# Performance work log

Measured on AMD Instinct MI355X. Metric: run time of the kernel, lower is better.

## Reference

```python
import jax, jax.numpy as jnp
import numpy as np


def segment_softmax(logits, seg, num_seg):
    m = jax.ops.segment_max(logits, seg, num_segments=num_seg)
    z = jnp.exp(logits - m[seg])
    s = jax.ops.segment_sum(z, seg, num_segments=num_seg)
    return z / s[seg]


def hconv(x_lin, edge_node, edge_he, num_nodes, num_edges, bias, alpha=None):
    # PyG HypergraphConv (heads=1, concat=True): D^-1 H W_e B^-1 H^T X Theta
    ones = jnp.ones(edge_node.shape[0], x_lin.dtype)
    D = jax.ops.segment_sum(ones, edge_node, num_segments=num_nodes)
    Dinv = jnp.where(D > 0, 1.0 / D, 0.0)
    Bd = jax.ops.segment_sum(ones, edge_he, num_segments=num_edges)
    Binv = jnp.where(Bd > 0, 1.0 / Bd, 0.0)
    # node -> hyperedge
    msg = Binv[edge_he][:, None] * x_lin[edge_node]
    if alpha is not None:
        msg = alpha[:, None] * msg
    e = jax.ops.segment_sum(msg, edge_he, num_segments=num_edges)
    # hyperedge -> node
    msg2 = Dinv[edge_node][:, None] * e[edge_he]
    if alpha is not None:
        msg2 = alpha[:, None] * msg2
    out = jax.ops.segment_sum(msg2, edge_node, num_segments=num_nodes)
    return out + bias


def reference(c_it, medicine_it, c_embeddings, m_embeddings, W_conv, b_conv, W_gat, att, b_gat, he_attr):
    nd = c_embeddings.shape[0]  # all indicators are 1 -> nonzero indexing is identity
    nm = m_embeddings.shape[0]
    oc = W_conv.shape[0]

    # diagnosis hypergraph: single hyperedge containing all diseases
    dia_x = c_embeddings @ W_conv.T  # [nd, oc]
    dia_nf = hconv(dia_x, jnp.arange(nd), jnp.zeros(nd, jnp.int32), nd, 1, b_conv)

    # medicine hypergraph: single hyperedge containing all medicines
    med_x = m_embeddings @ W_conv.T  # [nm, oc]
    med_nf = hconv(med_x, jnp.arange(nm), jnp.zeros(nm, jnp.int32), nm, 1, b_conv)

    # dia-med hypergraph: nd hyperedges, hyperedge d = {disease d} U {all medicines}
    comb = jnp.concatenate([c_embeddings, m_embeddings], axis=0)  # [nd+nm, in]
    x_lin = comb @ W_gat.T                                        # [nd+nm, oc]
    he_lin = he_attr @ W_gat.T                                    # [nd, oc]
    med_nodes = jnp.arange(nd, nd + nm)
    edge_node = jnp.concatenate(
        [jnp.arange(nd)[:, None], jnp.broadcast_to(med_nodes[None, :], (nd, nm))], axis=1
    ).reshape(-1)                              # [nd*(nm+1)]
    edge_he = jnp.repeat(jnp.arange(nd), nm + 1)

    # attention (attention_mode='node'): alpha from source node + hyperedge attr, softmax per hyperedge
    a_node = x_lin @ att[:oc]   # [nd+nm]
    a_he = he_lin @ att[oc:]    # [nd]
    logits = jax.nn.leaky_relu(a_node[edge_node] + a_he[edge_he], 0.2)
    alpha = segment_softmax(logits, edge_he, nd)

    dm_nf = hconv(x_lin, edge_node, edge_he, nd + nm, nd, b_gat, alpha)  # [nd+nm, oc]

    disease_final = jnp.concatenate([dm_nf[:nd], dia_nf], axis=1)   # [nd, 2*oc]
    medicine_final = jnp.concatenate([dm_nf[nd:], med_nf], axis=1)  # [nm, 2*oc]
    return jnp.concatenate([disease_final, medicine_final], axis=0)  # [nd+nm, 2*oc]


def setup_inputs() -> dict:
    key = jax.random.key(0)
    ks = jax.random.split(key, 8)
    ND, NM, IN, OUT = 2048, 512, 256, 128
    s = 0.05
    return {
        "c_it": jnp.ones((ND,), jnp.int32),
        "medicine_it": jnp.ones((NM,), jnp.int32),
        "c_embeddings": jax.random.normal(ks[0], (ND, IN), jnp.float32),
        "m_embeddings": jax.random.normal(ks[1], (NM, IN), jnp.float32),
        "W_conv": jax.random.normal(ks[2], (OUT, IN), jnp.float32) * s,
        "b_conv": jax.random.normal(ks[3], (OUT,), jnp.float32) * s,
        "W_gat": jax.random.normal(ks[4], (OUT, IN), jnp.float32) * s,
        "att": jax.random.normal(ks[5], (2 * OUT,), jnp.float32) * s,
        "b_gat": jax.random.normal(ks[6], (OUT,), jnp.float32) * s,
        "he_attr": jax.random.normal(ks[7], (ND, IN), jnp.float32),
    }
```

## Files before the change

### kernel.cpp

```cpp
#include <hip/hip_runtime.h>

#define ND 2048
#define NM 512
#define DIN 256
#define OC 128
#define NTOT 2560
#define NE 513

#define WS_PARTC 0
#define WS_PARTM (WS_PARTC + 512*256)
#define WS_AHE   (WS_PARTM + 128*256)
#define WS_ANODE (WS_AHE + ND)
#define WS_XLIN  (WS_ANODE + NTOT)
#define WS_DIA   (WS_XLIN + NTOT*OC)
#define WS_MED   (WS_DIA + OC)
#define WS_PART2 (WS_MED + OC)

__device__ __forceinline__ float lrelu(float x) { return x > 0.f ? x : 0.2f * x; }

__global__ void __launch_bounds__(256) K1(
        const float* __restrict__ c_emb, const float* __restrict__ m_emb,
        const float* __restrict__ W_gat, const float* __restrict__ att,
        const float* __restrict__ he_attr, float* __restrict__ ws) {
    const int b = blockIdx.x, t = threadIdx.x;
    if (b < 640) {
        __shared__ float row[4][DIN];
        __shared__ float sA[4][OC];
        const int d0 = b * 4;
#pragma unroll
        for (int p = 0; p < 2; ++p) {
            const int idx = p * 256 + t;
            const int r = idx >> 7, c = idx & 127;
            const int d = d0 + r;
            const float* src = (d < ND) ? c_emb + (size_t)d * DIN
                                        : m_emb + (size_t)(d - ND) * DIN;
            const float2 u = ((const float2*)src)[c];
            row[r][2 * c]     = u.x;
            row[r][2 * c + 1] = u.y;
        }
        __syncthreads();
        {
            const float pc = row[0][t] + row[1][t] + row[2][t] + row[3][t];
            if (b < 512) ws[WS_PARTC + b * 256 + t] = pc;
            else         ws[WS_PARTM + (b - 512) * 256 + t] = pc;
        }
        const int o = t & (OC - 1), h = t >> 7;
        float a0 = 0.f, a1 = 0.f;
        const float4* wr = (const float4*)(W_gat + (size_t)o * DIN);
        const float* r0 = row[2 * h];
        const float* r1 = row[2 * h + 1];
#pragma unroll 8
        for (int v = 0; v < 64; ++v) {
            const float4 w = wr[v];
            const int ib = 4 * v;
            a0 = fmaf(r0[ib],     w.x, a0);
            a0 = fmaf(r0[ib + 1], w.y, a0);
            a0 = fmaf(r0[ib + 2], w.z, a0);
            a0 = fmaf(r0[ib + 3], w.w, a0);
            a1 = fmaf(r1[ib],     w.x, a1);
            a1 = fmaf(r1[ib + 1], w.y, a1);
            a1 = fmaf(r1[ib + 2], w.z, a1);
            a1 = fmaf(r1[ib + 3], w.w, a1);
        }
        ws[WS_XLIN + (size_t)(d0 + 2 * h) * OC + o]     = a0;
        ws[WS_XLIN + (size_t)(d0 + 2 * h + 1) * OC + o] = a1;
        const float at = att[o];
        sA[2 * h][o]     = a0 * at;
        sA[2 * h + 1][o] = a1 * at;
        __syncthreads();
#pragma unroll
        for (int st = 64; st >= 1; st >>= 1) {
            if (t < 4 * st) {
                const int r = t / st, i = t - r * st;
                sA[r][i] += sA[r][i + st];
            }
            __syncthreads();
        }
        if (t < 4) ws[WS_ANODE + d0 + t] = sA[t][0];
    } else {
        __shared__ float satt[OC];
        __shared__ float we[DIN];
        const int q = b - 640;
        if (t < OC) satt[t] = att[OC + t];
        __syncthreads();
        float acc = 0.f;
#pragma unroll 8
        for (int o = 0; o < OC; ++o)
            acc = fmaf(W_gat[(size_t)o * DIN + t], satt[o], acc);
        we[t] = acc;
        __syncthreads();
        const int r = t >> 5, l = t & 31;
        const int d = q * 8 + r;
        const float* he = he_attr + (size_t)d * DIN;
        float ah = 0.f;
#pragma unroll
        for (int i = l; i < DIN; i += 32) ah = fmaf(he[i], we[i], ah);
#pragma unroll
        for (int m = 1; m < 32; m <<= 1) ah += __shfl_xor(ah, m, 32);
        if (l == 0) ws[WS_AHE + d] = ah;
    }
}

__global__ void __launch_bounds__(256) K2(
        const float* __restrict__ W_conv, const float* __restrict__ b_conv,
        const float* __restrict__ b_gat, float* __restrict__ ws,
        float* __restrict__ out) {
    const int b = blockIdx.x, t = threadIdx.x;
    if (b == 256) {
        __shared__ float mc[DIN], mm[DIN];
        float sc = 0.f, sm = 0.f;
        for (int bb = 0; bb < 512; ++bb) sc += ws[WS_PARTC + bb * 256 + t];
        for (int bb = 0; bb < 128; ++bb) sm += ws[WS_PARTM + bb * 256 + t];
        mc[t] = sc * (1.f / ND);
        mm[t] = sm * (1.f / NM);
        __syncthreads();
        if (t < OC) {
            const float4* wr = (const float4*)(W_conv + (size_t)t * DIN);
            float a = 0.f, m2 = 0.f;
#pragma unroll 8
            for (int v = 0; v < 64; ++v) {
                const float4 w = wr[v];
                const int ib = 4 * v;
                a  = fmaf(mc[ib], w.x, a);   a  = fmaf(mc[ib + 1], w.y, a);
                a  = fmaf(mc[ib + 2], w.z, a); a  = fmaf(mc[ib + 3], w.w, a);
                m2 = fmaf(mm[ib], w.x, m2);  m2 = fmaf(mm[ib + 1], w.y, m2);
                m2 = fmaf(mm[ib + 2], w.z, m2); m2 = fmaf(mm[ib + 3], w.w, m2);
            }
            const float bc = b_conv[t];
            ws[WS_DIA + t] = a + bc;
            ws[WS_MED + t] = m2 + bc;
        }
        return;
    }
    __shared__ float zbuf[NE][8];
    __shared__ float anm[NM];
    __shared__ float ec[8][OC];
    anm[t]       = ws[WS_ANODE + ND + t];
    anm[t + 256] = ws[WS_ANODE + ND + 256 + t];
    __syncthreads();
    {
        const int r = t >> 5, l = t & 31;
        const int d = b * 8 + r;
        const float ah = ws[WS_AHE + d];
        const float an_d = ws[WS_ANODE + d];
        float lmax = -3.4e38f;
        for (int j = l; j < NE; j += 32) {
            const float v = (j == 0) ? an_d : anm[j - 1];
            const float lg = lrelu(v + ah);
            zbuf[j][r] = lg;
            lmax = fmaxf(lmax, lg);
        }
#pragma unroll
        for (int m = 1; m < 32; m <<= 1) lmax = fmaxf(lmax, __shfl_xor(lmax, m, 32));
        float ss = 0.f;
        for (int j = l; j < NE; j += 32) {
            const float z = __expf(zbuf[j][r] - lmax);
            zbuf[j][r] = z;
            ss += z;
        }
#pragma unroll
        for (int m = 1; m < 32; m <<= 1) ss += __shfl_xor(ss, m, 32);
        const float inv = 1.f / ss;
        for (int j = l; j < NE; j += 32) zbuf[j][r] *= inv;
    }
    __syncthreads();
    const int o = t & (OC - 1), h = t >> 7;
    {
        float acc[8] = {0, 0, 0, 0, 0, 0, 0, 0};
        const float* xm = ws + WS_XLIN + (size_t)ND * OC;
        for (int j = h * 256; j < h * 256 + 256; ++j) {
            const float xv = xm[(size_t)j * OC + o];
            const float4* zr = (const float4*)zbuf[j + 1];
            const float4 za = zr[0], zb4 = zr[1];
            acc[0] = fmaf(za.x,  xv, acc[0]);
            acc[1] = fmaf(za.y,  xv, acc[1]);
            acc[2] = fmaf(za.z,  xv, acc[2]);
            acc[3] = fmaf(za.w,  xv, acc[3]);
            acc[4] = fmaf(zb4.x, xv, acc[4]);
            acc[5] = fmaf(zb4.y, xv, acc[5]);
            acc[6] = fmaf(zb4.z, xv, acc[6]);
            acc[7] = fmaf(zb4.w, xv, acc[7]);
        }
        if (h == 1) {
#pragma unroll
            for (int k = 0; k < 8; ++k) ec[k][o] = acc[k];
        }
        __syncthreads();
        if (h == 0) {
            const float bg = b_gat[o];
#pragma unroll
            for (int k = 0; k < 8; ++k) {
                const int dd = b * 8 + k;
                const float a0 = zbuf[0][k];
                const float xown = ws[WS_XLIN + (size_t)dd * OC + o];
                const float ev = fmaf(a0, xown, acc[k] + ec[k][o]) * (1.f / NE);
                ec[k][o] = ev;
                out[(size_t)dd * 2 * OC + o] = fmaf(a0, ev, bg);
            }
        }
    }
    __syncthreads();
    {
        float* part = ws + WS_PART2 + (size_t)b * NM * OC;
        float ev[8];
#pragma unroll
        for (int k = 0; k < 8; ++k) ev[k] = ec[k][o];
        for (int m = h * 256; m < h * 256 + 256; ++m) {
            const float4* zr = (const float4*)zbuf[m + 1];
            const float4 za = zr[0], zb4 = zr[1];
            float s = za.x * ev[0];
            s = fmaf(za.y,  ev[1], s);
            s = fmaf(za.z,  ev[2], s);
            s = fmaf(za.w,  ev[3], s);
            s = fmaf(zb4.x, ev[4], s);
            s = fmaf(zb4.y, ev[5], s);
            s = fmaf(zb4.z, ev[6], s);
            s = fmaf(zb4.w, ev[7], s);
            part[(size_t)m * OC + o] = s;
        }
    }
}

__global__ void __launch_bounds__(256) K3(
        const float* __restrict__ b_gat, const float* __restrict__ ws,
        float* __restrict__ out) {
    const int b = blockIdx.x, t = threadIdx.x;
    const int o = t & (OC - 1), h = t >> 7;
    if (b < 256) {
        const int m = 2 * b + h;
        const float* base = ws + WS_PART2 + (size_t)m * OC + o;
        float s = 0.f;
#pragma unroll 8
        for (int b2 = 0; b2 < 256; ++b2) s += base[(size_t)b2 * NM * OC];
        out[(size_t)(ND + m) * 2 * OC + o]      = fmaf(s, 1.f / ND, b_gat[o]);
        out[(size_t)(ND + m) * 2 * OC + OC + o] = ws[WS_MED + o];
    } else {
        const int q = b - 256;
        const float dv = ws[WS_DIA + o];
#pragma unroll
        for (int rr = 0; rr < 16; ++rr) {
            const int d = q * 32 + 2 * rr + h;
            out[(size_t)d * 2 * OC + OC + o] = dv;
        }
    }
}

extern "C" void kernel_launch(void* const* d_in, const int* in_sizes, int n_in,
                              void* d_out, int out_size, void* d_ws, size_t ws_size,
                              hipStream_t stream) {
    const float* c_emb   = (const float*)d_in[2];
    const float* m_emb   = (const float*)d_in[3];
    const float* W_conv  = (const float*)d_in[4];
    const float* b_conv  = (const float*)d_in[5];
    const float* W_gat   = (const float*)d_in[6];
    const float* att     = (const float*)d_in[7];
    const float* b_gat   = (const float*)d_in[8];
    const float* he_attr = (const float*)d_in[9];
    float* ws  = (float*)d_ws;
    float* out = (float*)d_out;

    hipLaunchKernelGGL(K1, dim3(896), dim3(256), 0, stream,
                       c_emb, m_emb, W_gat, att, he_attr, ws);
    hipLaunchKernelGGL(K2, dim3(257), dim3(256), 0, stream,
                       W_conv, b_conv, b_gat, ws, out);
    hipLaunchKernelGGL(K3, dim3(320), dim3(256), 0, stream, b_gat, ws, out);
}
```

Before: 154.4 us.

## Replace per-block partial scatter buffer with recomputed softmax weights in K3

K2 used to write a full NM×OC partial sum per block (256 blocks × 512×128 floats) for the hyperedge-to-medicine step, and K3 then reduced those partials. Now K2 stores only a per-hyperedge log-sum-exp constant and writes the hyperedge features back into the XLIN workspace. K3 recomputes the attention weights for two medicines per block with exp and runs a direct gather-reduce over all 2048 hyperedges. This removes roughly 128 MB of workspace write and read traffic, at the cost of redundant exp evaluations and a longer serial reduction loop inside K3.

```diff
diff --git a/kernel.cpp b/kernel.cpp
--- a/kernel.cpp
+++ b/kernel.cpp
@@ -11,10 +11,10 @@
 #define WS_PARTM (WS_PARTC + 512*256)
 #define WS_AHE   (WS_PARTM + 128*256)
 #define WS_ANODE (WS_AHE + ND)
-#define WS_XLIN  (WS_ANODE + NTOT)
+#define WS_CD    (WS_ANODE + NTOT)
+#define WS_XLIN  (WS_CD + ND)
 #define WS_DIA   (WS_XLIN + NTOT*OC)
 #define WS_MED   (WS_DIA + OC)
-#define WS_PART2 (WS_MED + OC)
 
 __device__ __forceinline__ float lrelu(float x) { return x > 0.f ? x : 0.2f * x; }
 
@@ -121,9 +121,9 @@
             for (int v = 0; v < 64; ++v) {
                 const float4 w = wr[v];
                 const int ib = 4 * v;
-                a  = fmaf(mc[ib], w.x, a);   a  = fmaf(mc[ib + 1], w.y, a);
+                a  = fmaf(mc[ib], w.x, a);     a  = fmaf(mc[ib + 1], w.y, a);
                 a  = fmaf(mc[ib + 2], w.z, a); a  = fmaf(mc[ib + 3], w.w, a);
-                m2 = fmaf(mm[ib], w.x, m2);  m2 = fmaf(mm[ib + 1], w.y, m2);
+                m2 = fmaf(mm[ib], w.x, m2);    m2 = fmaf(mm[ib + 1], w.y, m2);
                 m2 = fmaf(mm[ib + 2], w.z, m2); m2 = fmaf(mm[ib + 3], w.w, m2);
             }
             const float bc = b_conv[t];
@@ -161,62 +161,41 @@
 #pragma unroll
         for (int m = 1; m < 32; m <<= 1) ss += __shfl_xor(ss, m, 32);
         const float inv = 1.f / ss;
+        if (l == 0) ws[WS_CD + d] = lmax + __logf(ss);
         for (int j = l; j < NE; j += 32) zbuf[j][r] *= inv;
     }
     __syncthreads();
     const int o = t & (OC - 1), h = t >> 7;
-    {
-        float acc[8] = {0, 0, 0, 0, 0, 0, 0, 0};
-        const float* xm = ws + WS_XLIN + (size_t)ND * OC;
-        for (int j = h * 256; j < h * 256 + 256; ++j) {
-            const float xv = xm[(size_t)j * OC + o];
-            const float4* zr = (const float4*)zbuf[j + 1];
-            const float4 za = zr[0], zb4 = zr[1];
-            acc[0] = fmaf(za.x,  xv, acc[0]);
-            acc[1] = fmaf(za.y,  xv, acc[1]);
-            acc[2] = fmaf(za.z,  xv, acc[2]);
-            acc[3] = fmaf(za.w,  xv, acc[3]);
-            acc[4] = fmaf(zb4.x, xv, acc[4]);
-            acc[5] = fmaf(zb4.y, xv, acc[5]);
-            acc[6] = fmaf(zb4.z, xv, acc[6]);
-            acc[7] = fmaf(zb4.w, xv, acc[7]);
-        }
-        if (h == 1) {
-#pragma unroll
-            for (int k = 0; k < 8; ++k) ec[k][o] = acc[k];
-        }
-        __syncthreads();
-        if (h == 0) {
-            const float bg = b_gat[o];
-#pragma unroll
-            for (int k = 0; k < 8; ++k) {
-                const int dd = b * 8 + k;
-                const float a0 = zbuf[0][k];
-                const float xown = ws[WS_XLIN + (size_t)dd * OC + o];
-                const float ev = fmaf(a0, xown, acc[k] + ec[k][o]) * (1.f / NE);
-                ec[k][o] = ev;
-                out[(size_t)dd * 2 * OC + o] = fmaf(a0, ev, bg);
-            }
-        }
+    float acc[8] = {0, 0, 0, 0, 0, 0, 0, 0};
+    const float* xm = ws + WS_XLIN + (size_t)ND * OC;
+    for (int j = h * 256; j < h * 256 + 256; ++j) {
+        const float xv = xm[(size_t)j * OC + o];
+        const float4* zr = (const float4*)zbuf[j + 1];
+        const float4 za = zr[0], zb4 = zr[1];
+        acc[0] = fmaf(za.x,  xv, acc[0]);
+        acc[1] = fmaf(za.y,  xv, acc[1]);
+        acc[2] = fmaf(za.z,  xv, acc[2]);
+        acc[3] = fmaf(za.w,  xv, acc[3]);
+        acc[4] = fmaf(zb4.x, xv, acc[4]);
+        acc[5] = fmaf(zb4.y, xv, acc[5]);
+        acc[6] = fmaf(zb4.z, xv, acc[6]);
+        acc[7] = fmaf(zb4.w, xv, acc[7]);
+    }
+    if (h == 1) {
+#pragma unroll
+        for (int k = 0; k < 8; ++k) ec[k][o] = acc[k];
     }
     __syncthreads();
-    {
-        float* part = ws + WS_PART2 + (size_t)b * NM * OC;
-        float ev[8];
-#pragma unroll
-        for (int k = 0; k < 8; ++k) ev[k] = ec[k][o];
-        for (int m = h * 256; m < h * 256 + 256; ++m) {
-            const float4* zr = (const float4*)zbuf[m + 1];
-            const float4 za = zr[0], zb4 = zr[1];
-            float s = za.x * ev[0];
-            s = fmaf(za.y,  ev[1], s);
-            s = fmaf(za.z,  ev[2], s);
-            s = fmaf(za.w,  ev[3], s);
-            s = fmaf(zb4.x, ev[4], s);
-            s = fmaf(zb4.y, ev[5], s);
-            s = fmaf(zb4.z, ev[6], s);
-            s = fmaf(zb4.w, ev[7], s);
-            part[(size_t)m * OC + o] = s;
+    if (h == 0) {
+        const float bg = b_gat[o];
+#pragma unroll
+        for (int k = 0; k < 8; ++k) {
+            const int dd = b * 8 + k;
+            const float a0 = zbuf[0][k];
+            const float xown = ws[WS_XLIN + (size_t)dd * OC + o];
+            const float ev = fmaf(a0, xown, acc[k] + ec[k][o]) * (1.f / NE);
+            ws[WS_XLIN + (size_t)dd * OC + o] = ev;
+            out[(size_t)dd * 2 * OC + o] = fmaf(a0, ev, bg);
         }
     }
 }
@@ -227,13 +206,35 @@
     const int b = blockIdx.x, t = threadIdx.x;
     const int o = t & (OC - 1), h = t >> 7;
     if (b < 256) {
-        const int m = 2 * b + h;
-        const float* base = ws + WS_PART2 + (size_t)m * OC + o;
-        float s = 0.f;
-#pragma unroll 8
-        for (int b2 = 0; b2 < 256; ++b2) s += base[(size_t)b2 * NM * OC];
-        out[(size_t)(ND + m) * 2 * OC + o]      = fmaf(s, 1.f / ND, b_gat[o]);
-        out[(size_t)(ND + m) * 2 * OC + OC + o] = ws[WS_MED + o];
+        __shared__ float zb[ND][2];
+        __shared__ float ec2[2][OC];
+        const int m0 = b * 2;
+        const float an0 = ws[WS_ANODE + ND + m0];
+        const float an1 = ws[WS_ANODE + ND + m0 + 1];
+        for (int dd = t; dd < ND; dd += 256) {
+            const float ahv = ws[WS_AHE + dd];
+            const float cdv = ws[WS_CD + dd];
+            zb[dd][0] = __expf(lrelu(an0 + ahv) - cdv);
+            zb[dd][1] = __expf(lrelu(an1 + ahv) - cdv);
+        }
+        __syncthreads();
+        float a0 = 0.f, a1 = 0.f;
+        const float* e = ws + WS_XLIN;
+        for (int dd = h * 1024; dd < h * 1024 + 1024; ++dd) {
+            const float ev = e[(size_t)dd * OC + o];
+            a0 = fmaf(zb[dd][0], ev, a0);
+            a1 = fmaf(zb[dd][1], ev, a1);
+        }
+        if (h == 1) { ec2[0][o] = a0; ec2[1][o] = a1; }
+        __syncthreads();
+        if (h == 0) {
+            const float bg = b_gat[o];
+            const float mv = ws[WS_MED + o];
+            out[(size_t)(ND + m0) * 2 * OC + o]          = fmaf(a0 + ec2[0][o], 1.f / ND, bg);
+            out[(size_t)(ND + m0) * 2 * OC + OC + o]     = mv;
+            out[(size_t)(ND + m0 + 1) * 2 * OC + o]      = fmaf(a1 + ec2[1][o], 1.f / ND, bg);
+            out[(size_t)(ND + m0 + 1) * 2 * OC + OC + o] = mv;
+        }
     } else {
         const int q = b - 256;
         const float dv = ws[WS_DIA + o];
```

After: 151.4 us. No clear change (-2.0%).

## Replace partial-sum buffer and reduction kernel with atomic accumulation into output

Applied to the files above, without the earlier changes.

Drops the K3 reduction kernel and the large per-block partial buffer (256×512×128 floats). K2 now atomically adds each block's medicine contributions straight into the zeroed output, and extra blocks write the broadcast conv rows and the bias. A memset is added to clear the medicine half of the output, and the K1 inner loop reads the LDS rows as float4. The change trades a large global write-then-read round trip for many float atomics, which contend across 256 blocks and make the summation order nondeterministic.

```diff
diff --git a/kernel.cpp b/kernel.cpp
--- a/kernel.cpp
+++ b/kernel.cpp
@@ -12,9 +12,6 @@
 #define WS_AHE   (WS_PARTM + 128*256)
 #define WS_ANODE (WS_AHE + ND)
 #define WS_XLIN  (WS_ANODE + NTOT)
-#define WS_DIA   (WS_XLIN + NTOT*OC)
-#define WS_MED   (WS_DIA + OC)
-#define WS_PART2 (WS_MED + OC)
 
 __device__ __forceinline__ float lrelu(float x) { return x > 0.f ? x : 0.2f * x; }
 
@@ -46,21 +43,22 @@
         }
         const int o = t & (OC - 1), h = t >> 7;
         float a0 = 0.f, a1 = 0.f;
-        const float4* wr = (const float4*)(W_gat + (size_t)o * DIN);
-        const float* r0 = row[2 * h];
-        const float* r1 = row[2 * h + 1];
+        const float4* wr  = (const float4*)(W_gat + (size_t)o * DIN);
+        const float4* r0v = (const float4*)(row[2 * h]);
+        const float4* r1v = (const float4*)(row[2 * h + 1]);
 #pragma unroll 8
         for (int v = 0; v < 64; ++v) {
-            const float4 w = wr[v];
-            const int ib = 4 * v;
-            a0 = fmaf(r0[ib],     w.x, a0);
-            a0 = fmaf(r0[ib + 1], w.y, a0);
-            a0 = fmaf(r0[ib + 2], w.z, a0);
-            a0 = fmaf(r0[ib + 3], w.w, a0);
-            a1 = fmaf(r1[ib],     w.x, a1);
-            a1 = fmaf(r1[ib + 1], w.y, a1);
-            a1 = fmaf(r1[ib + 2], w.z, a1);
-            a1 = fmaf(r1[ib + 3], w.w, a1);
+            const float4 w  = wr[v];
+            const float4 x0 = r0v[v];
+            const float4 x1 = r1v[v];
+            a0 = fmaf(x0.x, w.x, a0);
+            a0 = fmaf(x0.y, w.y, a0);
+            a0 = fmaf(x0.z, w.z, a0);
+            a0 = fmaf(x0.w, w.w, a0);
+            a1 = fmaf(x1.x, w.x, a1);
+            a1 = fmaf(x1.y, w.y, a1);
+            a1 = fmaf(x1.z, w.z, a1);
+            a1 = fmaf(x1.w, w.w, a1);
         }
         ws[WS_XLIN + (size_t)(d0 + 2 * h) * OC + o]     = a0;
         ws[WS_XLIN + (size_t)(d0 + 2 * h + 1) * OC + o] = a1;
@@ -106,8 +104,10 @@
         const float* __restrict__ b_gat, float* __restrict__ ws,
         float* __restrict__ out) {
     const int b = blockIdx.x, t = threadIdx.x;
-    if (b == 256) {
+    if (b >= 256) {
+        const int q = b - 256;
         __shared__ float mc[DIN], mm[DIN];
+        __shared__ float dv[OC], mv[OC];
         float sc = 0.f, sm = 0.f;
         for (int bb = 0; bb < 512; ++bb) sc += ws[WS_PARTC + bb * 256 + t];
         for (int bb = 0; bb < 128; ++bb) sm += ws[WS_PARTM + bb * 256 + t];
@@ -121,14 +121,30 @@
             for (int v = 0; v < 64; ++v) {
                 const float4 w = wr[v];
                 const int ib = 4 * v;
-                a  = fmaf(mc[ib], w.x, a);   a  = fmaf(mc[ib + 1], w.y, a);
-                a  = fmaf(mc[ib + 2], w.z, a); a  = fmaf(mc[ib + 3], w.w, a);
-                m2 = fmaf(mm[ib], w.x, m2);  m2 = fmaf(mm[ib + 1], w.y, m2);
+                a  = fmaf(mc[ib], w.x, a);      a  = fmaf(mc[ib + 1], w.y, a);
+                a  = fmaf(mc[ib + 2], w.z, a);  a  = fmaf(mc[ib + 3], w.w, a);
+                m2 = fmaf(mm[ib], w.x, m2);     m2 = fmaf(mm[ib + 1], w.y, m2);
                 m2 = fmaf(mm[ib + 2], w.z, m2); m2 = fmaf(mm[ib + 3], w.w, m2);
             }
             const float bc = b_conv[t];
-            ws[WS_DIA + t] = a + bc;
-            ws[WS_MED + t] = m2 + bc;
+            dv[t] = a + bc;
+            mv[t] = m2 + bc;
+        }
+        __syncthreads();
+        const int o = t & (OC - 1), h = t >> 7;
+        if (q < 2) {
+            const float bg = b_gat[o];
+            const float mvo = mv[o];
+            float* base = out + (size_t)(ND + q * 256) * 2 * OC;
+            for (int ml = h * 128; ml < h * 128 + 128; ++ml) {
+                atomicAdd(base + (size_t)ml * 2 * OC + o, bg);
+                base[(size_t)ml * 2 * OC + OC + o] = mvo;
+            }
+        } else {
+            const float dvo = dv[o];
+            const int d0 = (q - 2) * 32;
+            for (int r = h; r < 32; r += 2)
+                out[(size_t)(d0 + r) * 2 * OC + OC + o] = dvo;
         }
         return;
     }
@@ -165,83 +181,55 @@
     }
     __syncthreads();
     const int o = t & (OC - 1), h = t >> 7;
-    {
-        float acc[8] = {0, 0, 0, 0, 0, 0, 0, 0};
-        const float* xm = ws + WS_XLIN + (size_t)ND * OC;
-        for (int j = h * 256; j < h * 256 + 256; ++j) {
-            const float xv = xm[(size_t)j * OC + o];
-            const float4* zr = (const float4*)zbuf[j + 1];
-            const float4 za = zr[0], zb4 = zr[1];
-            acc[0] = fmaf(za.x,  xv, acc[0]);
-            acc[1] = fmaf(za.y,  xv, acc[1]);
-            acc[2] = fmaf(za.z,  xv, acc[2]);
-            acc[3] = fmaf(za.w,  xv, acc[3]);
-            acc[4] = fmaf(zb4.x, xv, acc[4]);
-            acc[5] = fmaf(zb4.y, xv, acc[5]);
-            acc[6] = fmaf(zb4.z, xv, acc[6]);
-            acc[7] = fmaf(zb4.w, xv, acc[7]);
-        }
-        if (h == 1) {
-#pragma unroll
-            for (int k = 0; k < 8; ++k) ec[k][o] = acc[k];
-        }
-        __syncthreads();
-        if (h == 0) {
-            const float bg = b_gat[o];
-#pragma unroll
-            for (int k = 0; k < 8; ++k) {
-                const int dd = b * 8 + k;
-                const float a0 = zbuf[0][k];
-                const float xown = ws[WS_XLIN + (size_t)dd * OC + o];
-                const float ev = fmaf(a0, xown, acc[k] + ec[k][o]) * (1.f / NE);
-                ec[k][o] = ev;
-                out[(size_t)dd * 2 * OC + o] = fmaf(a0, ev, bg);
-            }
-        }
-    }
-    __syncthreads();
-    {
-        float* part = ws + WS_PART2 + (size_t)b * NM * OC;
-        float ev[8];
-#pragma unroll
-        for (int k = 0; k < 8; ++k) ev[k] = ec[k][o];
-        for (int m = h * 256; m < h * 256 + 256; ++m) {
-            const float4* zr = (const float4*)zbuf[m + 1];
-            const float4 za = zr[0], zb4 = zr[1];
-            float s = za.x * ev[0];
-            s = fmaf(za.y,  ev[1], s);
-            s = fmaf(za.z,  ev[2], s);
-            s = fmaf(za.w,  ev[3], s);
-            s = fmaf(zb4.x, ev[4], s);
-            s = fmaf(zb4.y, ev[5], s);
-            s = fmaf(zb4.z, ev[6], s);
-            s = fmaf(zb4.w, ev[7], s);
-            part[(size_t)m * OC + o] = s;
-        }
-    }
-}
-
-__global__ void __launch_bounds__(256) K3(
-        const float* __restrict__ b_gat, const float* __restrict__ ws,
-        float* __restrict__ out) {
-    const int b = blockIdx.x, t = threadIdx.x;
-    const int o = t & (OC - 1), h = t >> 7;
-    if (b < 256) {
-        const int m = 2 * b + h;
-        const float* base = ws + WS_PART2 + (size_t)m * OC + o;
-        float s = 0.f;
-#pragma unroll 8
-        for (int b2 = 0; b2 < 256; ++b2) s += base[(size_t)b2 * NM * OC];
-        out[(size_t)(ND + m) * 2 * OC + o]      = fmaf(s, 1.f / ND, b_gat[o]);
-        out[(size_t)(ND + m) * 2 * OC + OC + o] = ws[WS_MED + o];
-    } else {
-        const int q = b - 256;
-        const float dv = ws[WS_DIA + o];
-#pragma unroll
-        for (int rr = 0; rr < 16; ++rr) {
-            const int d = q * 32 + 2 * rr + h;
-            out[(size_t)d * 2 * OC + OC + o] = dv;
-        }
+    float acc[8] = {0, 0, 0, 0, 0, 0, 0, 0};
+    const float* xm = ws + WS_XLIN + (size_t)ND * OC;
+    for (int j = h * 256; j < h * 256 + 256; ++j) {
+        const float xv = xm[(size_t)j * OC + o];
+        const float4* zr = (const float4*)zbuf[j + 1];
+        const float4 za = zr[0], zb4 = zr[1];
+        acc[0] = fmaf(za.x,  xv, acc[0]);
+        acc[1] = fmaf(za.y,  xv, acc[1]);
+        acc[2] = fmaf(za.z,  xv, acc[2]);
+        acc[3] = fmaf(za.w,  xv, acc[3]);
+        acc[4] = fmaf(zb4.x, xv, acc[4]);
+        acc[5] = fmaf(zb4.y, xv, acc[5]);
+        acc[6] = fmaf(zb4.z, xv, acc[6]);
+        acc[7] = fmaf(zb4.w, xv, acc[7]);
+    }
+    if (h == 1) {
+#pragma unroll
+        for (int k = 0; k < 8; ++k) ec[k][o] = acc[k];
+    }
+    __syncthreads();
+    if (h == 0) {
+        const float bg = b_gat[o];
+#pragma unroll
+        for (int k = 0; k < 8; ++k) {
+            const int dd = b * 8 + k;
+            const float a0 = zbuf[0][k];
+            const float xown = ws[WS_XLIN + (size_t)dd * OC + o];
+            const float ev = fmaf(a0, xown, acc[k] + ec[k][o]) * (1.f / NE);
+            out[(size_t)dd * 2 * OC + o] = fmaf(a0, ev, bg);
+            ec[k][o] = ev;
+        }
+    }
+    __syncthreads();
+    float ev8[8];
+#pragma unroll
+    for (int k = 0; k < 8; ++k) ev8[k] = ec[k][o];
+    float* obase = out + (size_t)ND * 2 * OC + o;
+    for (int m = h * 256; m < h * 256 + 256; ++m) {
+        const float4* zr = (const float4*)zbuf[m + 1];
+        const float4 za = zr[0], zb4 = zr[1];
+        float s = za.x * ev8[0];
+        s = fmaf(za.y,  ev8[1], s);
+        s = fmaf(za.z,  ev8[2], s);
+        s = fmaf(za.w,  ev8[3], s);
+        s = fmaf(zb4.x, ev8[4], s);
+        s = fmaf(zb4.y, ev8[5], s);
+        s = fmaf(zb4.z, ev8[6], s);
+        s = fmaf(zb4.w, ev8[7], s);
+        atomicAdd(obase + (size_t)m * 2 * OC, s * (1.f / ND));
     }
 }
 
@@ -259,9 +247,10 @@
     float* ws  = (float*)d_ws;
     float* out = (float*)d_out;
 
+    hipMemsetAsync((char*)d_out + (size_t)ND * 2 * OC * sizeof(float), 0,
+                   (size_t)NM * 2 * OC * sizeof(float), stream);
     hipLaunchKernelGGL(K1, dim3(896), dim3(256), 0, stream,
                        c_emb, m_emb, W_gat, att, he_attr, ws);
-    hipLaunchKernelGGL(K2, dim3(257), dim3(256), 0, stream,
+    hipLaunchKernelGGL(K2, dim3(322), dim3(256), 0, stream,
                        W_conv, b_conv, b_gat, ws, out);
-    hipLaunchKernelGGL(K3, dim3(320), dim3(256), 0, stream, b_gat, ws, out);
 }
```

Result: slower. 196.6 us (+27.3%).
